# Optimization experiments

Measured on AMD Instinct MI355X. Metric: run time of the kernel, lower is better.

The kernel has to match this reference:

```python
import jax, jax.numpy as jnp
import numpy as np

EPS = 1e-8
LN_EPS = 1e-5
B, T, VDIM, ADIM, DM = 8, 2048, 1024, 768, 256
HID = 1024  # max(64, min(4*256, 2048))
DELTA_LOW, DELTA_HIGH = 2.0, 6.0
WINDOW = 5.0
GATE_MIN, GATE_MAX = 0.05, 0.95


def layer_norm(x):
    mu = jnp.mean(x, axis=-1, keepdims=True)
    var = jnp.var(x, axis=-1, keepdims=True)
    return (x - mu) / jnp.sqrt(var + LN_EPS)


def l2_normalize(x):
    n = jnp.sqrt(jnp.sum(x * x, axis=-1, keepdims=True))
    return x / jnp.maximum(n, EPS)


def setup_inputs() -> dict:
    key = jax.random.key(0)
    ks = jax.random.split(key, 8)
    inp = {
        "video_seq": jax.random.normal(ks[0], (B, T, VDIM), jnp.float32),
        "audio_seq": jax.random.normal(ks[1], (B, T, ADIM), jnp.float32),
        "Wv": jax.random.normal(ks[2], (VDIM, DM), jnp.float32) * (1.0 / np.sqrt(VDIM)),
        "bv": jnp.zeros((DM,), jnp.float32),
        "Wa": jax.random.normal(ks[3], (ADIM, DM), jnp.float32) * (1.0 / np.sqrt(ADIM)),
        "ba": jnp.zeros((DM,), jnp.float32),
        "theta": jnp.float32(0.0),
        "W1": jax.random.normal(ks[4], (3 * DM, HID), jnp.float32) * (1.0 / np.sqrt(3 * DM)),
        "b1": jnp.zeros((HID,), jnp.float32),
        "W2": jax.random.normal(ks[5], (HID, 1), jnp.float32) * (1.0 / np.sqrt(HID)),
        "b2": jnp.zeros((1,), jnp.float32),
    }
    return inp


def reference(video_seq, audio_seq, Wv, bv, Wa, ba, theta, W1, b1, W2, b2):
    v = layer_norm(video_seq @ Wv + bv)          # [B,T,DM]
    a = layer_norm(audio_seq @ Wa + ba)          # [B,T,DM]
    b, t, d = v.shape

    # LearnableDelay
    th = jnp.clip(theta, -12.0, 12.0)
    delta = DELTA_LOW + (DELTA_HIGH - DELTA_LOW) * jax.nn.sigmoid(th)
    delta_b = jnp.full((b,), delta, jnp.float32)

    # SoftTemporalShift (right shift with linear interpolation)
    dl = jnp.clip(delta_b, 0.0, float(t - 1))[:, None, None]   # [B,1,1]
    n = jnp.floor(dl)
    alpha = dl - n
    n_i = n.astype(jnp.int32)
    tidx = jnp.arange(t, dtype=jnp.int32)[None, :, None]       # [1,T,1]
    idx0 = jnp.clip(tidx - n_i, 0, t - 1)                      # [B,T,1]
    idx1 = jnp.clip(idx0 + 1, 0, t - 1)
    a0 = jnp.take_along_axis(a, jnp.broadcast_to(idx0, (b, t, d)), axis=1)
    a1 = jnp.take_along_axis(a, jnp.broadcast_to(idx1, (b, t, d)), axis=1)
    a_shift = (1.0 - alpha) * a0 + alpha * a1

    # DisplacementAwareCausalMask (hard, single scale)
    tf = jnp.arange(t, dtype=jnp.float32)
    tt = tf[None, :, None]                                     # t  -> [1,T,1]
    tau = tf[None, None, :]                                    # tau -> [1,1,T]
    center = jnp.minimum(jnp.maximum(tt + delta_b[:, None, None], 0.0), tt)
    raw = (jnp.abs(tau - center) <= WINDOW).astype(jnp.float32)
    raw = raw * (tau <= tt).astype(jnp.float32)
    M = raw / jnp.maximum(jnp.sum(raw, axis=-1, keepdims=True), EPS)  # [B,T,T]

    # mask-weighted audio context
    a_ctx = jnp.einsum('btk,bkd->btd', M, a_shift)

    # AlignmentGate (dropout inactive at eval)
    vn = l2_normalize(v)
    an = l2_normalize(a_ctx)
    x = jnp.concatenate([an, vn, an * vn], axis=-1)            # [B,T,3*DM]
    h = jax.nn.gelu(x @ W1 + b1, approximate=False)
    logits = jnp.clip(h @ W2 + b2, -12.0, 12.0)                # [B,T,1]
    g = jnp.clip(jax.nn.sigmoid(logits), GATE_MIN, GATE_MAX)

    fused = g * a_ctx + (1.0 - g) * v                          # [B,T,DM]
    return fused
```

## Files before the change

kernel.cpp:

```cpp
#include <hip/hip_runtime.h>
#include <cstdint>
#include <cstddef>

typedef unsigned short u16;
typedef unsigned int u32;
typedef __attribute__((ext_vector_type(8))) short short8;
typedef __attribute__((ext_vector_type(4))) float f32x4;

#define T_SEQ 2048
#define BT_ROWS 16384

__device__ __forceinline__ u16 f2bf(float x) {
  union { float f; u32 u; } v; v.f = x;
  u32 r = v.u + 0x7fffu + ((v.u >> 16) & 1u);
  return (u16)(r >> 16);
}
__device__ __forceinline__ u32 pkbf(float lo, float hi) {
  union { float f; u32 u; } a, b; a.f = lo; b.f = hi;
  const u32 ra = a.u + 0x7fffu + ((a.u >> 16) & 1u);
  const u32 rb = b.u + 0x7fffu + ((b.u >> 16) & 1u);
  return __builtin_amdgcn_perm(rb, ra, 0x07060302);
}
__device__ __forceinline__ float wave_bcast_sum(float x) {
#pragma unroll
  for (int off = 32; off > 0; off >>= 1) x += __shfl_down(x, off);
  return __shfl(x, 0);
}
__device__ __forceinline__ void gl_lds16(const void* g, void* l) {
  __builtin_amdgcn_global_load_lds((const __attribute__((address_space(1))) u32*)g,
                                   (__attribute__((address_space(3))) u32*)l, 16, 0, 0);
}
__device__ __forceinline__ float gelu_f(float x) {
  float z = 1.5957691216057308f * x * (1.0f + 0.044715f * x * x);
  float e = __expf(z);
  return x - x * __builtin_amdgcn_rcpf(1.0f + e);
}

__global__ __launch_bounds__(256) void tcvt_all(const float* __restrict__ Wv,
                                                const float* __restrict__ Wa,
                                                const float* __restrict__ W1,
                                                u16* __restrict__ wvT,
                                                u16* __restrict__ waT,
                                                u16* __restrict__ w1T,
                                                float* __restrict__ logits) {
  int b = blockIdx.x;
  if (b >= 1216) {
    logits[(b - 1216) * 256 + threadIdx.x] = 0.0f;
    return;
  }
  __shared__ float tile[32][33];
  const float* in; u16* out; int K, N, bx, by;
  if (b < 256)      { in = Wv; out = wvT; K = 1024; N = 256;  bx = b & 31;  by = b >> 5; }
  else if (b < 448) { b -= 256; in = Wa; out = waT; K = 768; N = 256;  bx = b % 24; by = b / 24; }
  else              { b -= 448; in = W1; out = w1T; K = 768; N = 1024; bx = b % 24; by = b / 24; }
  const int k0 = bx * 32, n0 = by * 32;
  const int tx = threadIdx.x & 31, ty = threadIdx.x >> 5;
#pragma unroll
  for (int r = 0; r < 4; r++)
    tile[ty + r * 8][tx] = in[(size_t)(k0 + ty + r * 8) * N + n0 + tx];
  __syncthreads();
#pragma unroll
  for (int r = 0; r < 4; r++)
    out[(size_t)(n0 + ty + r * 8) * K + k0 + tx] = f2bf(tile[tx][ty + r * 8]);
}

__global__ __launch_bounds__(256, 2) void proj_ln(const float* __restrict__ Vin,
                                                  const float* __restrict__ Ain,
                                                  const u16* __restrict__ wvT,
                                                  const u16* __restrict__ waT,
                                                  const float* __restrict__ bv,
                                                  const float* __restrict__ ba,
                                                  float* __restrict__ vOut,
                                                  float* __restrict__ aOut) {
  __shared__ __align__(16) u16 As[2][64 * 64];
  __shared__ __align__(16) u16 Bs[2][256 * 64];
  int b = blockIdx.x;
  const float* A; const u16* Bt; const float* bias; float* C; int K;
  if (b < 256) { A = Vin; Bt = wvT; bias = bv; C = vOut; K = 1024; }
  else         { b -= 256; A = Ain; Bt = waT; bias = ba; C = aOut; K = 768; }
  const int m0 = b * 64;
  const int tid = threadIdx.x;
  const int wave = tid >> 6, lane = tid & 63, qm = lane & 15, quad = lane >> 4;
  const int cw = wave * 64;

  const int ar = tid >> 2;
  const float* Arow = A + (size_t)(m0 + ar) * K + (tid & 3) * 4;
  int awAddr[4];
#pragma unroll
  for (int g = 0; g < 4; g++) {
    const int cg = ((tid & 3) >> 1) + 2 * g;
    awAddr[g] = ar * 64 + ((cg ^ (ar & 7)) * 8) + (tid & 1) * 4;
  }
  const int brow = tid >> 3;
  const int bpart = (tid & 7) ^ (brow & 7);
  const u16* Bp[8];
#pragma unroll
  for (int g = 0; g < 8; g++)
    Bp[g] = Bt + (size_t)(brow + g * 32) * K + bpart * 8;

  f32x4 acc[4][4] = {};

  {
    float4 p[4];
#pragma unroll
    for (int g = 0; g < 4; g++) p[g] = *(const float4*)(Arow + g * 16);
#pragma unroll
    for (int g = 0; g < 8; g++) gl_lds16(Bp[g], &Bs[0][(tid + g * 256) * 8]);
#pragma unroll
    for (int g = 0; g < 4; g++) {
      uint2 w; w.x = pkbf(p[g].x, p[g].y); w.y = pkbf(p[g].z, p[g].w);
      *(uint2*)&As[0][awAddr[g]] = w;
    }
  }
  __syncthreads();

  int cur = 0;
  for (int kt = 0; kt < K; kt += 64) {
    const int nxt = cur ^ 1;
    const int ktn = kt + 64;
    const bool more = ktn < K;
    float4 p[4];
    if (more) {
#pragma unroll
      for (int g = 0; g < 4; g++) p[g] = *(const float4*)(Arow + ktn + g * 16);
#pragma unroll
      for (int g = 0; g < 8; g++) gl_lds16(Bp[g] + ktn, &Bs[nxt][(tid + g * 256) * 8]);
    }
#pragma unroll
    for (int s = 0; s < 2; s++) {
      short8 af[4], bfr[4];
#pragma unroll
      for (int i = 0; i < 4; i++) {
        const int r = i * 16 + qm;
        af[i] = *(const short8*)&As[cur][r * 64 + ((s * 4 + quad) ^ (r & 7)) * 8];
      }
#pragma unroll
      for (int j = 0; j < 4; j++) {
        const int r = cw + j * 16 + qm;
        bfr[j] = *(const short8*)&Bs[cur][r * 64 + ((s * 4 + quad) ^ (r & 7)) * 8];
      }
#pragma unroll
      for (int i = 0; i < 4; i++)
#pragma unroll
        for (int j = 0; j < 4; j++)
          acc[i][j] = __builtin_amdgcn_mfma_f32_16x16x32_bf16(af[i], bfr[j], acc[i][j], 0, 0, 0);
    }
    if (more) {
#pragma unroll
      for (int g = 0; g < 4; g++) {
        uint2 w; w.x = pkbf(p[g].x, p[g].y); w.y = pkbf(p[g].z, p[g].w);
        *(uint2*)&As[nxt][awAddr[g]] = w;
      }
    }
    __syncthreads();
    cur = nxt;
  }

  float bcol[4];
#pragma unroll
  for (int j = 0; j < 4; j++) bcol[j] = bias[cw + j * 16 + qm];
#pragma unroll
  for (int i = 0; i < 4; i++)
#pragma unroll
    for (int j = 0; j < 4; j++)
#pragma unroll
      for (int r = 0; r < 4; r++)
        acc[i][j][r] += bcol[j];
  float s1[4][4], s2[4][4];
#pragma unroll
  for (int i = 0; i < 4; i++)
#pragma unroll
    for (int r = 0; r < 4; r++) {
      float a1 = 0, a2 = 0;
#pragma unroll
      for (int j = 0; j < 4; j++) { a1 += acc[i][j][r]; a2 += acc[i][j][r] * acc[i][j][r]; }
#pragma unroll
      for (int off = 1; off < 16; off <<= 1) {
        a1 += __shfl_xor(a1, off);
        a2 += __shfl_xor(a2, off);
      }
      s1[i][r] = a1; s2[i][r] = a2;
    }
  float* red = (float*)As;
  if (qm == 0) {
#pragma unroll
    for (int i = 0; i < 4; i++)
#pragma unroll
      for (int r = 0; r < 4; r++) {
        const int row = i * 16 + quad * 4 + r;
        red[row * 8 + wave * 2] = s1[i][r];
        red[row * 8 + wave * 2 + 1] = s2[i][r];
      }
  }
  __syncthreads();
#pragma unroll
  for (int i = 0; i < 4; i++)
#pragma unroll
    for (int r = 0; r < 4; r++) {
      const int row = i * 16 + quad * 4 + r;
      const float4 q1 = *(const float4*)&red[row * 8];
      const float4 q2 = *(const float4*)&red[row * 8 + 4];
      const float st = q1.x + q1.z + q2.x + q2.z;
      const float st2 = q1.y + q1.w + q2.y + q2.w;
      const float mu = st * (1.0f / 256.0f);
      const float var = st2 * (1.0f / 256.0f) - mu * mu;
      const float inv = rsqrtf(var + 1e-5f);
#pragma unroll
      for (int j = 0; j < 4; j++)
        C[(size_t)(m0 + row) * 256 + cw + j * 16 + qm] = (acc[i][j][r] - mu) * inv;
    }
}

__global__ __launch_bounds__(256, 3) void gemm_gelu_w2(const u16* __restrict__ Axb,
                                                       const u16* __restrict__ Bt,
                                                       const float* __restrict__ b1,
                                                       const float* __restrict__ W2,
                                                       float* __restrict__ logits) {
  constexpr int K = 768;
  __shared__ u16 As[128 * 64];
  __shared__ u16 Bs[128 * 64];
  const int tid = threadIdx.x;
  const int n0 = blockIdx.x * 128;
  const int m0 = blockIdx.y * 128;
  const int wave = tid >> 6, lane = tid & 63, qm = lane & 15, quad = lane >> 4;
  const int rw = (wave >> 1) * 64, cw = (wave & 1) * 64;

  const int crow = tid >> 3;
  const int cpart = (tid & 7) ^ (crow & 7);
  const u16* Ap[4];
  const u16* Bp[4];
#pragma unroll
  for (int g = 0; g < 4; g++) {
    Ap[g] = Axb + (size_t)(m0 + crow + g * 32) * K + cpart * 8;
    Bp[g] = Bt + (size_t)(n0 + crow + g * 32) * K + cpart * 8;
  }

  f32x4 acc[4][4] = {};
  for (int kt = 0; kt < K; kt += 64) {
#pragma unroll
    for (int g = 0; g < 4; g++) gl_lds16(Ap[g] + kt, &As[(tid + g * 256) * 8]);
#pragma unroll
    for (int g = 0; g < 4; g++) gl_lds16(Bp[g] + kt, &Bs[(tid + g * 256) * 8]);
    __syncthreads();
#pragma unroll
    for (int s = 0; s < 2; s++) {
      short8 af[4], bfr[4];
#pragma unroll
      for (int i = 0; i < 4; i++) {
        const int r = rw + i * 16 + qm;
        af[i] = *(const short8*)&As[r * 64 + ((s * 4 + quad) ^ (r & 7)) * 8];
      }
#pragma unroll
      for (int j = 0; j < 4; j++) {
        const int r = cw + j * 16 + qm;
        bfr[j] = *(const short8*)&Bs[r * 64 + ((s * 4 + quad) ^ (r & 7)) * 8];
      }
#pragma unroll
      for (int i = 0; i < 4; i++)
#pragma unroll
        for (int j = 0; j < 4; j++)
          acc[i][j] = __builtin_amdgcn_mfma_f32_16x16x32_bf16(af[i], bfr[j], acc[i][j], 0, 0, 0);
    }
    __syncthreads();
  }

  float w2j[4], bc[4];
#pragma unroll
  for (int j = 0; j < 4; j++) {
    const int col = n0 + cw + j * 16 + qm;
    w2j[j] = W2[col];
    bc[j] = b1[col];
  }
#pragma unroll
  for (int i = 0; i < 4; i++) {
#pragma unroll
    for (int r = 0; r < 4; r++) {
      float p = 0.0f;
#pragma unroll
      for (int j = 0; j < 4; j++)
        p += gelu_f(acc[i][j][r] + bc[j]) * w2j[j];
      p += __shfl_xor(p, 1);
      p += __shfl_xor(p, 2);
      p += __shfl_xor(p, 4);
      p += __shfl_xor(p, 8);
      if (qm == 0)
        atomicAdd(&logits[m0 + rw + i * 16 + quad * 4 + r], p);
    }
  }
}

__global__ __launch_bounds__(256) void shift_norm(const float* __restrict__ a,
                                                  const float* __restrict__ v,
                                                  float* __restrict__ actx,
                                                  u16* __restrict__ xb,
                                                  const float* __restrict__ theta) {
  const int row = blockIdx.x * 4 + (threadIdx.x >> 6);
  const int lane = threadIdx.x & 63;
  const int d4 = lane * 4;
  const int bb = row >> 11;
  const int t = row & (T_SEQ - 1);
  const float th = fminf(fmaxf(theta[0], -12.0f), 12.0f);
  const float delta = 2.0f + 4.0f * (1.0f / (1.0f + expf(-th)));
  const float dl = fminf(fmaxf(delta, 0.0f), (float)(T_SEQ - 1));
  const float nf = floorf(dl);
  const float alpha = dl - nf;
  const int ni = (int)nf;
  const float center = fminf(fmaxf((float)t + delta, 0.0f), (float)t);
  float sx = 0, sy = 0, sz = 0, sw = 0, cnt = 0.0f;
  const float* ab = a + (size_t)bb * T_SEQ * 256;
#pragma unroll
  for (int j = 0; j < 6; j++) {
    const int tau = t - 5 + j;
    if (tau < 0) continue;
    if (fabsf((float)tau - center) > 5.0f) continue;
    cnt += 1.0f;
    const int i0 = min(max(tau - ni, 0), T_SEQ - 1);
    const int i1 = min(i0 + 1, T_SEQ - 1);
    const float4 a0 = *(const float4*)&ab[(size_t)i0 * 256 + d4];
    const float4 a1 = *(const float4*)&ab[(size_t)i1 * 256 + d4];
    sx += a0.x + alpha * (a1.x - a0.x);
    sy += a0.y + alpha * (a1.y - a0.y);
    sz += a0.z + alpha * (a1.z - a0.z);
    sw += a0.w + alpha * (a1.w - a0.w);
  }
  const float sc = 1.0f / fmaxf(cnt, 1e-8f);
  float4 o; o.x = sx * sc; o.y = sy * sc; o.z = sz * sc; o.w = sw * sc;
  *(float4*)&actx[(size_t)row * 256 + d4] = o;
  const float4 vv = *(const float4*)&v[(size_t)row * 256 + d4];
  float sa2 = o.x * o.x + o.y * o.y + o.z * o.z + o.w * o.w;
  float sv2 = vv.x * vv.x + vv.y * vv.y + vv.z * vv.z + vv.w * vv.w;
  sa2 = wave_bcast_sum(sa2);
  sv2 = wave_bcast_sum(sv2);
  const float ia = 1.0f / fmaxf(sqrtf(sa2), 1e-8f);
  const float iv = 1.0f / fmaxf(sqrtf(sv2), 1e-8f);
  const float anx = o.x * ia, any_ = o.y * ia, anz = o.z * ia, anw = o.w * ia;
  const float vnx = vv.x * iv, vny = vv.y * iv, vnz = vv.z * iv, vnw = vv.w * iv;
  u16* xr = xb + (size_t)row * 768;
  u32 pa[2] = {pkbf(anx, any_), pkbf(anz, anw)};
  u32 pv[2] = {pkbf(vnx, vny), pkbf(vnz, vnw)};
  u32 pp[2] = {pkbf(anx * vnx, any_ * vny), pkbf(anz * vnz, anw * vnw)};
  *(uint2*)&xr[d4] = *(uint2*)pa;
  *(uint2*)&xr[256 + d4] = *(uint2*)pv;
  *(uint2*)&xr[512 + d4] = *(uint2*)pp;
}

__global__ __launch_bounds__(256) void gate_mix(const float* __restrict__ logits,
                                                const float* __restrict__ b2,
                                                const float* __restrict__ actx,
                                                const float* __restrict__ v,
                                                float* __restrict__ out) {
  const int row = blockIdx.x * 4 + (threadIdx.x >> 6);
  const int lane = threadIdx.x & 63;
  const float l = fminf(fmaxf(logits[row] + b2[0], -12.0f), 12.0f);
  float g = 1.0f / (1.0f + expf(-l));
  g = fminf(fmaxf(g, 0.05f), 0.95f);
  const float4 aa = *(const float4*)&actx[(size_t)row * 256 + lane * 4];
  const float4 vv = *(const float4*)&v[(size_t)row * 256 + lane * 4];
  float4 o;
  o.x = g * aa.x + (1.0f - g) * vv.x;
  o.y = g * aa.y + (1.0f - g) * vv.y;
  o.z = g * aa.z + (1.0f - g) * vv.z;
  o.w = g * aa.w + (1.0f - g) * vv.w;
  *(float4*)&out[(size_t)row * 256 + lane * 4] = o;
}

extern "C" void kernel_launch(void* const* d_in, const int* in_sizes, int n_in,
                              void* d_out, int out_size, void* d_ws, size_t ws_size,
                              hipStream_t stream) {
  const float* video = (const float*)d_in[0];
  const float* audio = (const float*)d_in[1];
  const float* Wv    = (const float*)d_in[2];
  const float* bv    = (const float*)d_in[3];
  const float* Wa    = (const float*)d_in[4];
  const float* ba    = (const float*)d_in[5];
  const float* theta = (const float*)d_in[6];
  const float* W1    = (const float*)d_in[7];
  const float* b1    = (const float*)d_in[8];
  const float* W2    = (const float*)d_in[9];
  const float* b2    = (const float*)d_in[10];
  float* out = (float*)d_out;
  char* ws = (char*)d_ws;

  const size_t OFF_WVT = 0;
  const size_t OFF_WAT = 524288;
  const size_t OFF_W1T = 917504;
  const size_t OFF_LOG = 2490368;
  const size_t OFF_V   = 2555904;
  const size_t OFF_A   = 19333120;
  const size_t OFF_ACTX= 36110336;
  const size_t OFF_XB  = 52887552;

  u16* wvT = (u16*)(ws + OFF_WVT);
  u16* waT = (u16*)(ws + OFF_WAT);
  u16* w1T = (u16*)(ws + OFF_W1T);
  float* logits = (float*)(ws + OFF_LOG);
  float* v    = (float*)(ws + OFF_V);
  float* a    = (float*)(ws + OFF_A);
  float* actx = (float*)(ws + OFF_ACTX);
  u16* xb = (u16*)(ws + OFF_XB);

  tcvt_all<<<1280, 256, 0, stream>>>(Wv, Wa, W1, wvT, waT, w1T, logits);
  proj_ln<<<512, 256, 0, stream>>>(video, audio, wvT, waT, bv, ba, v, a);
  shift_norm<<<BT_ROWS / 4, 256, 0, stream>>>(a, v, actx, xb, theta);
  gemm_gelu_w2<<<dim3(8, BT_ROWS / 128), 256, 0, stream>>>(xb, w1T, b1, W2, logits);
  gate_mix<<<BT_ROWS / 4, 256, 0, stream>>>(logits, b2, actx, v, out);
}
```

Baseline: 244.3 us.

## Load projection weight fragments directly into registers, drop B LDS staging

The projection+LayerNorm kernel no longer stages the transposed weight tile in shared memory. Each wave loads its MFMA B fragments straight from global memory into double-buffered registers, with K made a compile-time template parameter so the loop can be fully unrolled. It also uses a barrier that waits only on LDS counters, and raises wave priority around the MFMA block. This cuts shared-memory footprint and LDS traffic, which may allow more blocks per CU, at the cost of more registers and uncoalesced, repeated global reads of the weights across blocks.

```diff
diff --git a/kernel.cpp b/kernel.cpp
--- a/kernel.cpp
+++ b/kernel.cpp
@@ -34,6 +34,10 @@
   float z = 1.5957691216057308f * x * (1.0f + 0.044715f * x * x);
   float e = __expf(z);
   return x - x * __builtin_amdgcn_rcpf(1.0f + e);
+}
+__device__ __forceinline__ void lgkm_barrier() {
+  asm volatile("s_waitcnt lgkmcnt(0)" ::: "memory");
+  __builtin_amdgcn_s_barrier();
 }
 
 __global__ __launch_bounds__(256) void tcvt_all(const float* __restrict__ Wv,
@@ -64,6 +68,144 @@
     out[(size_t)(n0 + ty + r * 8) * K + k0 + tx] = f2bf(tile[tx][ty + r * 8]);
 }
 
+template <int K>
+__device__ __forceinline__ void proj_body(const float* __restrict__ A,
+                                          const u16* __restrict__ Bt,
+                                          const float* __restrict__ bias,
+                                          float* __restrict__ C,
+                                          int m0, u16* As) {
+  constexpr int NT = K / 64;
+  const int tid = threadIdx.x;
+  const int wave = tid >> 6, lane = tid & 63, qm = lane & 15, quad = lane >> 4;
+  const int cw = wave * 64;
+
+  const int ar = tid >> 2;
+  const float* Arow = A + (size_t)(m0 + ar) * K + (tid & 3) * 4;
+  int awAddr[4];
+#pragma unroll
+  for (int g = 0; g < 4; g++) {
+    const int cg = ((tid & 3) >> 1) + 2 * g;
+    awAddr[g] = ar * 64 + ((cg ^ (ar & 7)) * 8) + (tid & 1) * 4;
+  }
+  const u16* brow[4];
+#pragma unroll
+  for (int j = 0; j < 4; j++)
+    brow[j] = Bt + (size_t)(cw + j * 16 + qm) * K + quad * 8;
+
+  f32x4 acc[4][4] = {};
+  short8 bfrag[2][8];
+  float4 p[4];
+
+#pragma unroll
+  for (int g = 0; g < 4; g++) p[g] = *(const float4*)(Arow + g * 16);
+#pragma unroll
+  for (int s = 0; s < 2; s++)
+#pragma unroll
+    for (int j = 0; j < 4; j++)
+      bfrag[0][s * 4 + j] = *(const short8*)(brow[j] + s * 32);
+#pragma unroll
+  for (int g = 0; g < 4; g++) {
+    uint2 w; w.x = pkbf(p[g].x, p[g].y); w.y = pkbf(p[g].z, p[g].w);
+    *(uint2*)&As[awAddr[g]] = w;
+  }
+  lgkm_barrier();
+
+#pragma unroll
+  for (int t = 0; t < NT; t++) {
+    const int cb = t & 1, nb = cb ^ 1;
+    if (t + 1 < NT) {
+#pragma unroll
+      for (int g = 0; g < 4; g++)
+        p[g] = *(const float4*)(Arow + (t + 1) * 64 + g * 16);
+#pragma unroll
+      for (int s = 0; s < 2; s++)
+#pragma unroll
+        for (int j = 0; j < 4; j++)
+          bfrag[nb][s * 4 + j] = *(const short8*)(brow[j] + (t + 1) * 64 + s * 32);
+    }
+#pragma unroll
+    for (int s = 0; s < 2; s++) {
+      short8 af[4];
+#pragma unroll
+      for (int i = 0; i < 4; i++) {
+        const int r = i * 16 + qm;
+        af[i] = *(const short8*)&As[cb * 4096 + r * 64 + ((s * 4 + quad) ^ (r & 7)) * 8];
+      }
+      __builtin_amdgcn_s_setprio(1);
+#pragma unroll
+      for (int i = 0; i < 4; i++)
+#pragma unroll
+        for (int j = 0; j < 4; j++)
+          acc[i][j] = __builtin_amdgcn_mfma_f32_16x16x32_bf16(
+              af[i], bfrag[cb][s * 4 + j], acc[i][j], 0, 0, 0);
+      __builtin_amdgcn_s_setprio(0);
+    }
+    if (t + 1 < NT) {
+#pragma unroll
+      for (int g = 0; g < 4; g++) {
+        uint2 w; w.x = pkbf(p[g].x, p[g].y); w.y = pkbf(p[g].z, p[g].w);
+        *(uint2*)&As[nb * 4096 + awAddr[g]] = w;
+      }
+      lgkm_barrier();
+    }
+  }
+
+  float bcol[4];
+#pragma unroll
+  for (int j = 0; j < 4; j++) bcol[j] = bias[cw + j * 16 + qm];
+#pragma unroll
+  for (int i = 0; i < 4; i++)
+#pragma unroll
+    for (int j = 0; j < 4; j++)
+#pragma unroll
+      for (int r = 0; r < 4; r++)
+        acc[i][j][r] += bcol[j];
+  float s1[4][4], s2[4][4];
+#pragma unroll
+  for (int i = 0; i < 4; i++)
+#pragma unroll
+    for (int r = 0; r < 4; r++) {
+      float a1 = 0, a2 = 0;
+#pragma unroll
+      for (int j = 0; j < 4; j++) { a1 += acc[i][j][r]; a2 += acc[i][j][r] * acc[i][j][r]; }
+#pragma unroll
+      for (int off = 1; off < 16; off <<= 1) {
+        a1 += __shfl_xor(a1, off);
+        a2 += __shfl_xor(a2, off);
+      }
+      s1[i][r] = a1; s2[i][r] = a2;
+    }
+  __syncthreads();
+  float* red = (float*)As;
+  if (qm == 0) {
+#pragma unroll
+    for (int i = 0; i < 4; i++)
+#pragma unroll
+      for (int r = 0; r < 4; r++) {
+        const int row = i * 16 + quad * 4 + r;
+        red[row * 8 + wave * 2] = s1[i][r];
+        red[row * 8 + wave * 2 + 1] = s2[i][r];
+      }
+  }
+  __syncthreads();
+#pragma unroll
+  for (int i = 0; i < 4; i++)
+#pragma unroll
+    for (int r = 0; r < 4; r++) {
+      const int row = i * 16 + quad * 4 + r;
+      const float4 q1 = *(const float4*)&red[row * 8];
+      const float4 q2 = *(const float4*)&red[row * 8 + 4];
+      const float st = q1.x + q1.z + q2.x + q2.z;
+      const float st2 = q1.y + q1.w + q2.y + q2.w;
+      const float mu = st * (1.0f / 256.0f);
+      const float var = st2 * (1.0f / 256.0f) - mu * mu;
+      const float inv = rsqrtf(var + 1e-5f);
+#pragma unroll
+      for (int j = 0; j < 4; j++)
+        C[(size_t)(m0 + row) * 256 + cw + j * 16 + qm] = (acc[i][j][r] - mu) * inv;
+    }
+}
+
 __global__ __launch_bounds__(256, 2) void proj_ln(const float* __restrict__ Vin,
                                                   const float* __restrict__ Ain,
                                                   const u16* __restrict__ wvT,
@@ -73,142 +215,11 @@
                                                   float* __restrict__ vOut,
                                                   float* __restrict__ aOut) {
   __shared__ __align__(16) u16 As[2][64 * 64];
-  __shared__ __align__(16) u16 Bs[2][256 * 64];
   int b = blockIdx.x;
-  const float* A; const u16* Bt; const float* bias; float* C; int K;
-  if (b < 256) { A = Vin; Bt = wvT; bias = bv; C = vOut; K = 1024; }
-  else         { b -= 256; A = Ain; Bt = waT; bias = ba; C = aOut; K = 768; }
-  const int m0 = b * 64;
-  const int tid = threadIdx.x;
-  const int wave = tid >> 6, lane = tid & 63, qm = lane & 15, quad = lane >> 4;
-  const int cw = wave * 64;
-
-  const int ar = tid >> 2;
-  const float* Arow = A + (size_t)(m0 + ar) * K + (tid & 3) * 4;
-  int awAddr[4];
-#pragma unroll
-  for (int g = 0; g < 4; g++) {
-    const int cg = ((tid & 3) >> 1) + 2 * g;
-    awAddr[g] = ar * 64 + ((cg ^ (ar & 7)) * 8) + (tid & 1) * 4;
-  }
-  const int brow = tid >> 3;
-  const int bpart = (tid & 7) ^ (brow & 7);
-  const u16* Bp[8];
-#pragma unroll
-  for (int g = 0; g < 8; g++)
-    Bp[g] = Bt + (size_t)(brow + g * 32) * K + bpart * 8;
-
-  f32x4 acc[4][4] = {};
-
-  {
-    float4 p[4];
-#pragma unroll
-    for (int g = 0; g < 4; g++) p[g] = *(const float4*)(Arow + g * 16);
-#pragma unroll
-    for (int g = 0; g < 8; g++) gl_lds16(Bp[g], &Bs[0][(tid + g * 256) * 8]);
-#pragma unroll
-    for (int g = 0; g < 4; g++) {
-      uint2 w; w.x = pkbf(p[g].x, p[g].y); w.y = pkbf(p[g].z, p[g].w);
-      *(uint2*)&As[0][awAddr[g]] = w;
-    }
-  }
-  __syncthreads();
-
-  int cur = 0;
-  for (int kt = 0; kt < K; kt += 64) {
-    const int nxt = cur ^ 1;
-    const int ktn = kt + 64;
-    const bool more = ktn < K;
-    float4 p[4];
-    if (more) {
-#pragma unroll
-      for (int g = 0; g < 4; g++) p[g] = *(const float4*)(Arow + ktn + g * 16);
-#pragma unroll
-      for (int g = 0; g < 8; g++) gl_lds16(Bp[g] + ktn, &Bs[nxt][(tid + g * 256) * 8]);
-    }
-#pragma unroll
-    for (int s = 0; s < 2; s++) {
-      short8 af[4], bfr[4];
-#pragma unroll
-      for (int i = 0; i < 4; i++) {
-        const int r = i * 16 + qm;
-        af[i] = *(const short8*)&As[cur][r * 64 + ((s * 4 + quad) ^ (r & 7)) * 8];
-      }
-#pragma unroll
-      for (int j = 0; j < 4; j++) {
-        const int r = cw + j * 16 + qm;
-        bfr[j] = *(const short8*)&Bs[cur][r * 64 + ((s * 4 + quad) ^ (r & 7)) * 8];
-      }
-#pragma unroll
-      for (int i = 0; i < 4; i++)
-#pragma unroll
-        for (int j = 0; j < 4; j++)
-          acc[i][j] = __builtin_amdgcn_mfma_f32_16x16x32_bf16(af[i], bfr[j], acc[i][j], 0, 0, 0);
-    }
-    if (more) {
-#pragma unroll
-      for (int g = 0; g < 4; g++) {
-        uint2 w; w.x = pkbf(p[g].x, p[g].y); w.y = pkbf(p[g].z, p[g].w);
-        *(uint2*)&As[nxt][awAddr[g]] = w;
-      }
-    }
-    __syncthreads();
-    cur = nxt;
-  }
-
-  float bcol[4];
-#pragma unroll
-  for (int j = 0; j < 4; j++) bcol[j] = bias[cw + j * 16 + qm];
-#pragma unroll
-  for (int i = 0; i < 4; i++)
-#pragma unroll
-    for (int j = 0; j < 4; j++)
-#pragma unroll
-      for (int r = 0; r < 4; r++)
-        acc[i][j][r] += bcol[j];
-  float s1[4][4], s2[4][4];
-#pragma unroll
-  for (int i = 0; i < 4; i++)
-#pragma unroll
-    for (int r = 0; r < 4; r++) {
-      float a1 = 0, a2 = 0;
-#pragma unroll
-      for (int j = 0; j < 4; j++) { a1 += acc[i][j][r]; a2 += acc[i][j][r] * acc[i][j][r]; }
-#pragma unroll
-      for (int off = 1; off < 16; off <<= 1) {
-        a1 += __shfl_xor(a1, off);
-        a2 += __shfl_xor(a2, off);
-      }
-      s1[i][r] = a1; s2[i][r] = a2;
-    }
-  float* red = (float*)As;
-  if (qm == 0) {
-#pragma unroll
-    for (int i = 0; i < 4; i++)
-#pragma unroll
-      for (int r = 0; r < 4; r++) {
-        const int row = i * 16 + quad * 4 + r;
-        red[row * 8 + wave * 2] = s1[i][r];
-        red[row * 8 + wave * 2 + 1] = s2[i][r];
-      }
-  }
-  __syncthreads();
-#pragma unroll
-  for (int i = 0; i < 4; i++)
-#pragma unroll
-    for (int r = 0; r < 4; r++) {
-      const int row = i * 16 + quad * 4 + r;
-      const float4 q1 = *(const float4*)&red[row * 8];
-      const float4 q2 = *(const float4*)&red[row * 8 + 4];
-      const float st = q1.x + q1.z + q2.x + q2.z;
-      const float st2 = q1.y + q1.w + q2.y + q2.w;
-      const float mu = st * (1.0f / 256.0f);
-      const float var = st2 * (1.0f / 256.0f) - mu * mu;
-      const float inv = rsqrtf(var + 1e-5f);
-#pragma unroll
-      for (int j = 0; j < 4; j++)
-        C[(size_t)(m0 + row) * 256 + cw + j * 16 + qm] = (acc[i][j][r] - mu) * inv;
-    }
+  if (b < 256)
+    proj_body<1024>(Vin, wvT, bv, vOut, b * 64, &As[0][0]);
+  else
+    proj_body<768>(Ain, waT, ba, aOut, (b - 256) * 64, &As[0][0]);
 }
 
 __global__ __launch_bounds__(256, 3) void gemm_gelu_w2(const u16* __restrict__ Axb,
```

Result: no change. 246.1 us (+0.7%).
